# Optimization experiments

Measured on AMD Instinct MI355X. Metric: run time of the kernel, lower is better.

Reference implementation:

```python
import jax, jax.numpy as jnp
import numpy as np

N_NODES = 50000
N_EDGES = 800000
NUM_GRAPHS = 256
F_IN = 64        # num_features (per-head out dim == in dim in this module)
HEADS = 4        # n_heads1
OUT_DIM = 128    # output_dim
HC = HEADS * F_IN
NEG_SLOPE = 0.2  # GATConv leaky_relu slope
EPS = 1e-5       # GraphNorm eps


def setup_inputs() -> dict:
    key = jax.random.key(0)
    ks = jax.random.split(key, 12)
    s = lambda k, shape, fan: (jax.random.normal(k, shape, jnp.float32) / np.sqrt(fan).astype(np.float32))
    return {
        "x": jax.random.normal(ks[0], (N_NODES, F_IN), jnp.float32),
        "edge_index": jax.random.randint(ks[1], (2, N_EDGES), 0, N_NODES),
        "batch": jnp.sort(jax.random.randint(ks[2], (N_NODES,), 0, NUM_GRAPHS)),
        # GATConv params
        "lin_w": s(ks[3], (HC, F_IN), F_IN),
        "att_src": s(ks[4], (HEADS, F_IN), F_IN),
        "att_dst": s(ks[5], (HEADS, F_IN), F_IN),
        "gat_bias": jnp.zeros((HC,), jnp.float32),
        # GraphNorm params
        "gn_weight": jnp.ones((HC,), jnp.float32),
        "gn_bias": jnp.zeros((HC,), jnp.float32),
        "gn_mean_scale": jnp.ones((HC,), jnp.float32),
        # fc_g1 / out heads
        "fc1_w": s(ks[6], (OUT_DIM, HC), HC), "fc1_b": jnp.zeros((OUT_DIM,), jnp.float32),
        "out_w": s(ks[7], (1, OUT_DIM), OUT_DIM), "out_b": jnp.zeros((1,), jnp.float32),
        # GlobalAttention gate_nn: Linear(HC,16) -> ReLU -> Linear(16,1) -> Sigmoid
        "att1_w": s(ks[8], (16, HC), HC), "att1_b": jnp.zeros((16,), jnp.float32),
        "att2_w": s(ks[9], (1, 16), 16), "att2_b": jnp.zeros((1,), jnp.float32),
    }


def _gat_conv(x, edge_index, lin_w, att_src, att_dst, gat_bias):
    """PyG GATConv with add_self_loops=True, concat heads. Returns (out [N,HC], alpha [E+N,H])."""
    N = x.shape[0]
    xh = (x @ lin_w.T).reshape(N, HEADS, F_IN)                 # [N,H,C]
    a_src = (xh * att_src[None]).sum(-1)                        # [N,H]
    a_dst = (xh * att_dst[None]).sum(-1)                        # [N,H]
    loops = jnp.arange(N)
    src = jnp.concatenate([edge_index[0], loops])               # [E+N]
    dst = jnp.concatenate([edge_index[1], loops])
    alpha = jax.nn.leaky_relu(a_src[src] + a_dst[dst], NEG_SLOPE)  # [E+N,H]
    # segment softmax over incoming edges of each dst node (self-loops guarantee non-empty)
    amax = jax.ops.segment_max(alpha, dst, num_segments=N)
    alpha = jnp.exp(alpha - amax[dst])
    denom = jax.ops.segment_sum(alpha, dst, num_segments=N)
    alpha = alpha / (denom[dst] + 1e-16)
    msg = xh[src] * alpha[:, :, None]                           # [E+N,H,C]
    out = jax.ops.segment_sum(msg, dst, num_segments=N).reshape(N, HC) + gat_bias
    return out, alpha


def _graph_norm(x, batch, weight, bias, mean_scale):
    ones = jnp.ones((x.shape[0],), x.dtype)
    cnt = jnp.maximum(jax.ops.segment_sum(ones, batch, num_segments=NUM_GRAPHS), 1.0)[:, None]
    mean = jax.ops.segment_sum(x, batch, num_segments=NUM_GRAPHS) / cnt
    sub = x - mean[batch] * mean_scale
    var = jax.ops.segment_sum(sub * sub, batch, num_segments=NUM_GRAPHS) / cnt
    return weight * sub / jnp.sqrt(var + EPS)[batch] + bias


def _global_attention(x, batch, att1_w, att1_b, att2_w, att2_b):
    gate = jax.nn.sigmoid(jax.nn.relu(x @ att1_w.T + att1_b) @ att2_w.T + att2_b)  # [N,1]
    gmax = jax.ops.segment_max(gate, batch, num_segments=NUM_GRAPHS)
    gate = jnp.exp(gate - gmax[batch])
    gden = jax.ops.segment_sum(gate, batch, num_segments=NUM_GRAPHS)
    gate = gate / (gden[batch] + 1e-16)
    return jax.ops.segment_sum(gate * x, batch, num_segments=NUM_GRAPHS)  # [G,HC]


def reference(x, edge_index, batch, lin_w, att_src, att_dst, gat_bias,
              gn_weight, gn_bias, gn_mean_scale, fc1_w, fc1_b, out_w, out_b,
              att1_w, att1_b, att2_w, att2_b):
    x2, alpha = _gat_conv(x, edge_index, lin_w, att_src, att_dst, gat_bias)
    h = _graph_norm(x2, batch, gn_weight, gn_bias, gn_mean_scale)
    h = jax.nn.relu(h)                                # node_dropout = identity (eval)
    pooled = _global_attention(h, batch, att1_w, att1_b, att2_w, att2_b)
    h = jax.nn.relu(pooled @ fc1_w.T + fc1_b)          # dropout = identity (eval)
    out = jax.nn.sigmoid(h @ out_w.T + out_b)          # [G,1]
    return out, alpha
```

## Files before the change

### kernel.cpp

```cpp
#include <hip/hip_runtime.h>
#include <hip/hip_fp16.h>
#include <math.h>

#define NN 50000
#define NE 800000
#define NG 256
#define NEG_SLOPE 0.2f
#define GEPS 1e-5f
#define CHUNK 64
#define NB 196
#define CAP 6144
#define NAB 261
#define EPB 3072
#define NLINB 782
#define ABLK 3321
#define GMAX 512

typedef _Float16 f16x8 __attribute__((ext_vector_type(8)));
typedef _Float16 f16x4 __attribute__((ext_vector_type(4)));
typedef float f32x4 __attribute__((ext_vector_type(4)));
typedef float f32x2 __attribute__((ext_vector_type(2)));

__device__ __forceinline__ float lrelu(float v){ return v > 0.f ? v : NEG_SLOPE * v; }

__global__ __launch_bounds__(256) void k_misc(const float* __restrict__ lin_w,
                                              _Float16* __restrict__ wh,
                                              const float* __restrict__ att1_w,
                                              _Float16* __restrict__ a1w,
                                              const int* __restrict__ batch,
                                              int* __restrict__ goff,
                                              int* __restrict__ gcnt,
                                              int* __restrict__ bucket_cnt) {
  int b = blockIdx.x, tid = threadIdx.x;
  if (b == 0) {
    if (tid < NB) bucket_cnt[tid] = 0;
    int g = tid;
    int lo = 0, hi = NN;
    while (lo < hi) { int mid = (lo + hi) >> 1; if (batch[mid] < g) lo = mid + 1; else hi = mid; }
    int start = lo;
    lo = 0; hi = NN;
    while (lo < hi) { int mid = (lo + hi) >> 1; if (batch[mid] < g + 1) lo = mid + 1; else hi = mid; }
    goff[g] = start;
    gcnt[g] = lo - start;
  } else if (b <= 16) {
    int i0 = (b - 1) * 1024 + tid * 4;
    float4 f = *(const float4*)&lin_w[i0];
    f16x4 h4;
    h4[0] = (_Float16)f.x; h4[1] = (_Float16)f.y; h4[2] = (_Float16)f.z; h4[3] = (_Float16)f.w;
    *(f16x4*)&wh[i0] = h4;
  } else {
    int i0 = (b - 17) * 1024 + tid * 4;
    float4 f = *(const float4*)&att1_w[i0];
    f16x4 h4;
    h4[0] = (_Float16)f.x; h4[1] = (_Float16)f.y; h4[2] = (_Float16)f.z; h4[3] = (_Float16)f.w;
    *(f16x4*)&a1w[i0] = h4;
  }
}

__device__ __forceinline__ void lin_body(char* smem,
                                         const float* __restrict__ x,
                                         const _Float16* __restrict__ wh,
                                         const float* __restrict__ att_src,
                                         const float* __restrict__ att_dst,
                                         unsigned char* __restrict__ xh8,
                                         float* __restrict__ a_src_n,
                                         float* __restrict__ a_dst_n) {
  unsigned char* s_f8 = (unsigned char*)smem;
  int w = threadIdx.x >> 6, lane = threadIdx.x & 63;
  int nb = blockIdx.x * 64 + w * 16;
  if (nb >= NN) return;
  int am = lane & 15, quad = lane >> 4;
  int wb = w * 4096;

  const float* xr = x + (size_t)(nb + am) * 64 + quad * 8;
  float4 f0 = *(const float4*)(xr);
  float4 f1 = *(const float4*)(xr + 4);
  float4 f2 = *(const float4*)(xr + 32);
  float4 f3 = *(const float4*)(xr + 36);
  f16x8 a0, a1;
  a0[0] = (_Float16)f0.x; a0[1] = (_Float16)f0.y; a0[2] = (_Float16)f0.z; a0[3] = (_Float16)f0.w;
  a0[4] = (_Float16)f1.x; a0[5] = (_Float16)f1.y; a0[6] = (_Float16)f1.z; a0[7] = (_Float16)f1.w;
  a1[0] = (_Float16)f2.x; a1[1] = (_Float16)f2.y; a1[2] = (_Float16)f2.z; a1[3] = (_Float16)f2.w;
  a1[4] = (_Float16)f3.x; a1[5] = (_Float16)f3.y; a1[6] = (_Float16)f3.z; a1[7] = (_Float16)f3.w;

  f32x4 acc[16];
#pragma unroll
  for (int ct = 0; ct < 16; ct++) acc[ct] = (f32x4){0.f, 0.f, 0.f, 0.f};

#pragma unroll
  for (int ct = 0; ct < 16; ct++) {
    const _Float16* wbp = wh + (size_t)(ct * 16 + am) * 64 + quad * 8;
    f16x8 b0 = *(const f16x8*)(wbp);
    f16x8 b1 = *(const f16x8*)(wbp + 32);
    acc[ct] = __builtin_amdgcn_mfma_f32_16x16x32_f16(a0, b0, acc[ct], 0, 0, 0);
    acc[ct] = __builtin_amdgcn_mfma_f32_16x16x32_f16(a1, b1, acc[ct], 0, 0, 0);
  }

  float ps[4][4], pd[4][4];
#pragma unroll
  for (int r = 0; r < 4; r++)
#pragma unroll
    for (int h = 0; h < 4; h++) { ps[r][h] = 0.f; pd[r][h] = 0.f; }
#pragma unroll
  for (int ct = 0; ct < 16; ct++) {
    int c = ct * 16 + am;
    float av = att_src[c];
    float dv = att_dst[c];
    int h = ct >> 2;
#pragma unroll
    for (int r = 0; r < 4; r++) {
      float v = acc[ct][r];
      ps[r][h] += v * av;
      pd[r][h] += v * dv;
    }
  }
#pragma unroll
  for (int r = 0; r < 4; r++)
#pragma unroll
    for (int h = 0; h < 4; h++) {
      float s = ps[r][h], d = pd[r][h];
#pragma unroll
      for (int o = 1; o < 16; o <<= 1) {
        s += __shfl_xor(s, o, 64);
        d += __shfl_xor(d, o, 64);
      }
      if (am == 0) {
        int node = nb + quad * 4 + r;
        a_src_n[node * 4 + h] = s;
        a_dst_n[node * 4 + h] = d;
      }
    }

#pragma unroll
  for (int r = 0; r < 4; r++) {
    uint4 u;
    int t;
    t = __builtin_amdgcn_cvt_pk_fp8_f32(acc[0][r],  acc[1][r],  0, 0);
    t = __builtin_amdgcn_cvt_pk_fp8_f32(acc[2][r],  acc[3][r],  t, 1);
    u.x = (unsigned)t;
    t = __builtin_amdgcn_cvt_pk_fp8_f32(acc[4][r],  acc[5][r],  0, 0);
    t = __builtin_amdgcn_cvt_pk_fp8_f32(acc[6][r],  acc[7][r],  t, 1);
    u.y = (unsigned)t;
    t = __builtin_amdgcn_cvt_pk_fp8_f32(acc[8][r],  acc[9][r],  0, 0);
    t = __builtin_amdgcn_cvt_pk_fp8_f32(acc[10][r], acc[11][r], t, 1);
    u.z = (unsigned)t;
    t = __builtin_amdgcn_cvt_pk_fp8_f32(acc[12][r], acc[13][r], 0, 0);
    t = __builtin_amdgcn_cvt_pk_fp8_f32(acc[14][r], acc[15][r], t, 1);
    u.w = (unsigned)t;
    *(uint4*)&s_f8[wb + (quad * 4 + r) * 256 + am * 16] = u;
  }
#pragma unroll
  for (int p = 0; p < 4; p++) {
    uint4 u = *(const uint4*)&s_f8[wb + p * 1024 + lane * 16];
    *(uint4*)&xh8[(size_t)nb * 256 + p * 1024 + lane * 16] = u;
  }
}

__device__ __forceinline__ void binA_body(char* smem, int b,
                                          const int* __restrict__ ei,
                                          int* __restrict__ bucket_cnt,
                                          int2* __restrict__ ebuf) {
  int2* sorted = (int2*)smem;
  int*  hist   = (int*)(smem + 24576);
  int*  lbase  = (int*)(smem + 25360);
  int*  cur    = (int*)(smem + 26144);
  int*  runb   = (int*)(smem + 26928);
  int*  wsum   = (int*)(smem + 27712);
  int tid = threadIdx.x, lane = tid & 63, wid = tid >> 6;
  int e0 = b * EPB, e1 = min(e0 + EPB, NE);
  int n = e1 - e0;
  bool full = (e0 + EPB <= NE);

  int dd[12];
  if (full) {
#pragma unroll
    for (int r = 0; r < 3; r++) {
      int e = e0 + r * 1024 + tid * 4;
      int4 v = *(const int4*)&ei[NE + e];
      dd[r * 4 + 0] = v.x; dd[r * 4 + 1] = v.y;
      dd[r * 4 + 2] = v.z; dd[r * 4 + 3] = v.w;
    }
  } else {
#pragma unroll
    for (int r = 0; r < 3; r++)
#pragma unroll
      for (int k = 0; k < 4; k++) {
        int e = e0 + r * 1024 + tid * 4 + k;
        dd[r * 4 + k] = (e < e1) ? ei[NE + e] : -1;
      }
  }
  if (tid < NB) hist[tid] = 0;
  __syncthreads();
#pragma unroll
  for (int q = 0; q < 12; q++)
    if (dd[q] >= 0) atomicAdd(&hist[dd[q] >> 8], 1);
  __syncthreads();
  {
    int v = (tid < NB) ? hist[tid] : 0;
    int s = v;
#pragma unroll
    for (int o = 1; o < 64; o <<= 1) { int t = __shfl_up(s, o, 64); if (lane >= o) s += t; }
    if (lane == 63) wsum[wid] = s;
    __syncthreads();
    int wbase = 0;
    for (int k = 0; k < wid; k++) wbase += wsum[k];
    if (tid < NB) {
      int ex = wbase + s - v;
      lbase[tid] = ex;
      cur[tid] = ex;
      runb[tid] = atomicAdd(&bucket_cnt[tid], v);
    }
  }
  __syncthreads();
  int ss[12];
  if (full) {
#pragma unroll
    for (int r = 0; r < 3; r++) {
      int e = e0 + r * 1024 + tid * 4;
      int4 v = *(const int4*)&ei[e];
      ss[r * 4 + 0] = v.x; ss[r * 4 + 1] = v.y;
      ss[r * 4 + 2] = v.z; ss[r * 4 + 3] = v.w;
    }
  } else {
#pragma unroll
    for (int r = 0; r < 3; r++)
#pragma unroll
      for (int k = 0; k < 4; k++) {
        int e = e0 + r * 1024 + tid * 4 + k;
        ss[r * 4 + k] = (e < e1) ? ei[e] : 0;
      }
  }
#pragma unroll
  for (int q = 0; q < 12; q++) {
    int d = dd[q];
    if (d >= 0) {
      int lp = atomicAdd(&cur[d >> 8], 1);
      sorted[lp] = make_int2(d, ss[q]);
    }
  }
  __syncthreads();
  for (int i = tid; i < n; i += 256) {
    int2 e = sorted[i];
    int bk = e.x >> 8;
    int slot = runb[bk] + (i - lbase[bk]);
    if (slot < CAP) ebuf[(size_t)bk * CAP + slot] = e;
  }
}

__global__ __launch_bounds__(256) void k_linbin(const float* __restrict__ x,
                                                const _Float16* __restrict__ wh,
                                                const float* __restrict__ att_src,
                                                const float* __restrict__ att_dst,
                                                unsigned char* __restrict__ xh8,
                                                float* __restrict__ a_src_n,
                                                float* __restrict__ a_dst_n,
                                                const int* __restrict__ ei,
                                                int* __restrict__ bucket_cnt,
                                                int2* __restrict__ ebuf) {
  __shared__ __align__(16) char smem[27744];
  if (blockIdx.x < NLINB)
    lin_body(smem, x, wh, att_src, att_dst, xh8, a_src_n, a_dst_n);
  else
    binA_body(smem, blockIdx.x - NLINB, ei, bucket_cnt, ebuf);
}

__global__ __launch_bounds__(256) void k_binB(const int2* __restrict__ ebuf,
                                              const int* __restrict__ bucket_cnt,
                                              int* __restrict__ deg,
                                              int* __restrict__ offs,
                                              int* __restrict__ src_list) {
  __shared__ int hist[256];
  __shared__ int cur[256];
  __shared__ int wsum[4];
  __shared__ int bbase[NB];
  int b = blockIdx.x, tid = threadIdx.x, lane = tid & 63, wid = tid >> 6;
  {
    int v = (tid < NB) ? min(bucket_cnt[tid], CAP) : 0;
    int s = v;
#pragma unroll
    for (int o = 1; o < 64; o <<= 1) { int t = __shfl_up(s, o, 64); if (lane >= o) s += t; }
    if (lane == 63) wsum[wid] = s;
    __syncthreads();
    int wbase = 0;
    for (int k = 0; k < wid; k++) wbase += wsum[k];
    if (tid < NB) bbase[tid] = wbase + s - v;
  }
  __syncthreads();
  int cnt = min(bucket_cnt[b], CAP);
  int base = bbase[b];
  const int2* seg = ebuf + (size_t)b * CAP;
  hist[tid] = 0;
  __syncthreads();
  for (int i = tid; i < cnt; i += 256) atomicAdd(&hist[seg[i].x & 255], 1);
  __syncthreads();
  int v = hist[tid];
  int s = v;
#pragma unroll
  for (int o = 1; o < 64; o <<= 1) { int t = __shfl_up(s, o, 64); if (lane >= o) s += t; }
  if (lane == 63) wsum[wid] = s;
  __syncthreads();
  int wbase = 0;
  for (int k = 0; k < wid; k++) wbase += wsum[k];
  int excl = wbase + s - v;
  int node = b * 256 + tid;
  if (node < NN) {
    deg[node] = v;
    offs[node] = base + excl;
  }
  cur[tid] = excl;
  __syncthreads();
  for (int i = tid; i < cnt; i += 256) {
    int2 e = seg[i];
    int pos = base + atomicAdd(&cur[e.x & 255], 1);
    src_list[pos] = e.y;
  }
}

__global__ __launch_bounds__(64) void k_gat(const unsigned char* __restrict__ xh8,
                                            const float* __restrict__ a_src_n,
                                            const float* __restrict__ a_dst_n,
                                            const int* __restrict__ offs,
                                            const int* __restrict__ deg_arr,
                                            const int* __restrict__ src_list,
                                            const float* __restrict__ gat_bias,
                                            __half* __restrict__ x2h,
                                            float* __restrict__ den_inv) {
  __shared__ __align__(16) float s_al[CHUNK * 4];
  __shared__ int s_src[CHUNK];
  __shared__ __half s_tr[256];
  int n = blockIdx.x, lane = threadIdx.x;
  int off = offs[n], dg = deg_arr[n], cnt = dg + 1;
  float4 ad = *(const float4*)&a_dst_n[n * 4];
  int h = lane & 3;
  unsigned loff = 4u * (unsigned)lane;
  float acc0 = 0.f, acc1 = 0.f, acc2 = 0.f, acc3 = 0.f;

  if (cnt <= 64) {
    float e0 = 0.f, e1 = 0.f, e2 = 0.f, e3 = 0.f;
    if (lane < cnt) {
      int src = (lane < dg) ? src_list[off + lane] : n;
      float4 as = *(const float4*)&a_src_n[src * 4];
      e0 = __expf(lrelu(as.x + ad.x));
      e1 = __expf(lrelu(as.y + ad.y));
      e2 = __expf(lrelu(as.z + ad.z));
      e3 = __expf(lrelu(as.w + ad.w));
      s_src[lane] = src;
    }
    float s0 = e0, s1 = e1, s2 = e2, s3 = e3;
#pragma unroll
    for (int o = 32; o >= 1; o >>= 1) {
      s0 += __shfl_xor(s0, o, 64);
      s1 += __shfl_xor(s1, o, 64);
      s2 += __shfl_xor(s2, o, 64);
      s3 += __shfl_xor(s3, o, 64);
    }
    float i0 = 1.f / (s0 + 1e-16f), i1 = 1.f / (s1 + 1e-16f);
    float i2 = 1.f / (s2 + 1e-16f), i3 = 1.f / (s3 + 1e-16f);
    if (lane == 0) *(float4*)&den_inv[n * 4] = make_float4(i0, i1, i2, i3);
    if (lane < cnt) {
      s_al[lane * 4 + 0] = e0 * i0;
      s_al[lane * 4 + 1] = e1 * i1;
      s_al[lane * 4 + 2] = e2 * i2;
      s_al[lane * 4 + 3] = e3 * i3;
    }
    __syncthreads();
    int j = 0;
    for (; j + 4 <= cnt; j += 4) {
      unsigned oA = ((unsigned)s_src[j] << 8) + loff;
      unsigned oB = ((unsigned)s_src[j + 1] << 8) + loff;
      unsigned oC = ((unsigned)s_src[j + 2] << 8) + loff;
      unsigned oD = ((unsigned)s_src[j + 3] << 8) + loff;
      unsigned rA = *(const unsigned*)&xh8[oA];
      unsigned rB = *(const unsigned*)&xh8[oB];
      unsigned rC = *(const unsigned*)&xh8[oC];
      unsigned rD = *(const unsigned*)&xh8[oD];
      float aA = s_al[j * 4 + h], aB = s_al[(j + 1) * 4 + h];
      float aC = s_al[(j + 2) * 4 + h], aD = s_al[(j + 3) * 4 + h];
      f32x2 lA = __builtin_amdgcn_cvt_pk_f32_fp8((int)rA, 0);
      f32x2 hA = __builtin_amdgcn_cvt_pk_f32_fp8((int)rA, 1);
      f32x2 lB = __builtin_amdgcn_cvt_pk_f32_fp8((int)rB, 0);
      f32x2 hB = __builtin_amdgcn_cvt_pk_f32_fp8((int)rB, 1);
      f32x2 lC = __builtin_amdgcn_cvt_pk_f32_fp8((int)rC, 0);
      f32x2 hC = __builtin_amdgcn_cvt_pk_f32_fp8((int)rC, 1);
      f32x2 lD = __builtin_amdgcn_cvt_pk_f32_fp8((int)rD, 0);
      f32x2 hD = __builtin_amdgcn_cvt_pk_f32_fp8((int)rD, 1);
      acc0 += aA * lA[0] + aB * lB[0] + aC * lC[0] + aD * lD[0];
      acc1 += aA * lA[1] + aB * lB[1] + aC * lC[1] + aD * lD[1];
      acc2 += aA * hA[0] + aB * hB[0] + aC * hC[0] + aD * hD[0];
      acc3 += aA * hA[1] + aB * hB[1] + aC * hC[1] + aD * hD[1];
    }
    for (; j < cnt; j++) {
      unsigned oA = ((unsigned)s_src[j] << 8) + loff;
      unsigned rA = *(const unsigned*)&xh8[oA];
      float aA = s_al[j * 4 + h];
      f32x2 lA = __builtin_amdgcn_cvt_pk_f32_fp8((int)rA, 0);
      f32x2 hA = __builtin_amdgcn_cvt_pk_f32_fp8((int)rA, 1);
      acc0 += aA * lA[0];
      acc1 += aA * lA[1];
      acc2 += aA * hA[0];
      acc3 += aA * hA[1];
    }
  } else {
    float s0 = 0.f, s1 = 0.f, s2 = 0.f, s3 = 0.f;
    for (int j = lane; j < cnt; j += 64) {
      int src = (j < dg) ? src_list[off + j] : n;
      float4 as = *(const float4*)&a_src_n[src * 4];
      s0 += __expf(lrelu(as.x + ad.x));
      s1 += __expf(lrelu(as.y + ad.y));
      s2 += __expf(lrelu(as.z + ad.z));
      s3 += __expf(lrelu(as.w + ad.w));
    }
#pragma unroll
    for (int o = 32; o >= 1; o >>= 1) {
      s0 += __shfl_xor(s0, o, 64);
      s1 += __shfl_xor(s1, o, 64);
      s2 += __shfl_xor(s2, o, 64);
      s3 += __shfl_xor(s3, o, 64);
    }
    float i0 = 1.f / (s0 + 1e-16f), i1 = 1.f / (s1 + 1e-16f);
    float i2 = 1.f / (s2 + 1e-16f), i3 = 1.f / (s3 + 1e-16f);
    if (lane == 0) *(float4*)&den_inv[n * 4] = make_float4(i0, i1, i2, i3);
    for (int cb = 0; cb < cnt; cb += CHUNK) {
      int clen = min(CHUNK, cnt - cb);
      for (int j = lane; j < clen; j += 64) {
        int jj = cb + j;
        int src = (jj < dg) ? src_list[off + jj] : n;
        float4 as = *(const float4*)&a_src_n[src * 4];
        s_src[j] = src;
        s_al[j * 4 + 0] = __expf(lrelu(as.x + ad.x)) * i0;
        s_al[j * 4 + 1] = __expf(lrelu(as.y + ad.y)) * i1;
        s_al[j * 4 + 2] = __expf(lrelu(as.z + ad.z)) * i2;
        s_al[j * 4 + 3] = __expf(lrelu(as.w + ad.w)) * i3;
      }
      __syncthreads();
      for (int j = 0; j < clen; j++) {
        unsigned oA = ((unsigned)s_src[j] << 8) + loff;
        unsigned rA = *(const unsigned*)&xh8[oA];
        float aA = s_al[j * 4 + h];
        f32x2 lA = __builtin_amdgcn_cvt_pk_f32_fp8((int)rA, 0);
        f32x2 hA = __builtin_amdgcn_cvt_pk_f32_fp8((int)rA, 1);
        acc0 += aA * lA[0];
        acc1 += aA * lA[1];
        acc2 += aA * hA[0];
        acc3 += aA * hA[1];
      }
      __syncthreads();
    }
  }

  int cb0 = (lane & 3) * 64 + (lane >> 2);
  s_tr[cb0 +  0] = __float2half(acc0 + gat_bias[cb0 +  0]);
  s_tr[cb0 + 16] = __float2half(acc1 + gat_bias[cb0 + 16]);
  s_tr[cb0 + 32] = __float2half(acc2 + gat_bias[cb0 + 32]);
  s_tr[cb0 + 48] = __float2half(acc3 + gat_bias[cb0 + 48]);
  __syncthreads();
  uint2 u = *(const uint2*)&s_tr[4 * lane];
  *(uint2*)&x2h[(size_t)n * 256 + 4 * lane] = u;
}

__global__ __launch_bounds__(256) void k_tail(const int* __restrict__ ei,
                                              const float* __restrict__ a_src_n,
                                              const float* __restrict__ a_dst_n,
                                              const float* __restrict__ den_inv,
                                              float* __restrict__ alpha_out,
                                              const int* __restrict__ gcnt,
                                              const int* __restrict__ goff,
                                              const float* __restrict__ gn_w,
                                              const float* __restrict__ gn_b,
                                              const float* __restrict__ gn_ms,
                                              const __half* __restrict__ x2h,
                                              const _Float16* __restrict__ a1w,
                                              const float* __restrict__ att1_b,
                                              const float* __restrict__ att2_w,
                                              const float* __restrict__ att2_b,
                                              const float* __restrict__ fc1_w,
                                              const float* __restrict__ fc1_b,
                                              const float* __restrict__ out_w,
                                              const float* __restrict__ out_b,
                                              float* __restrict__ outp) {
  if (blockIdx.x >= NG) {
    int idx = (blockIdx.x - NG) * 256 + threadIdx.x;
    if (idx >= NE + NN) return;
    int s, d;
    if (idx < NE) { s = ei[idx]; d = ei[NE + idx]; }
    else          { s = idx - NE; d = s; }
    float4 as = *(const float4*)&a_src_n[s * 4];
    float4 ad = *(const float4*)&a_dst_n[d * 4];
    float4 iv = *(const float4*)&den_inv[d * 4];
    float4 a;
    a.x = __expf(lrelu(as.x + ad.x)) * iv.x;
    a.y = __expf(lrelu(as.y + ad.y)) * iv.y;
    a.z = __expf(lrelu(as.z + ad.z)) * iv.z;
    a.w = __expf(lrelu(as.w + ad.w)) * iv.w;
    *(float4*)&alpha_out[(size_t)idx * 4] = a;
    return;
  }

  __shared__ __align__(16) float s_sc[256];
  __shared__ __align__(16) float s_sh[256];
  __shared__ float s_gate[GMAX];
  __shared__ __align__(16) float pool_s[256];
  __shared__ float hred[128];
  __shared__ float red[4];
  int g = blockIdx.x, tid = threadIdx.x, lane = tid & 63, wid = tid >> 6;
  int cnt = gcnt[g], start = goff[g];

  {
    int c = tid;
    const __half* p = x2h + (size_t)start * 256 + c;
    float S = 0.f, S2 = 0.f;
    int i = 0;
    for (; i + 7 < cnt; i += 8) {
      float v0 = __half2float(p[(size_t)(i + 0) * 256]);
      float v1 = __half2float(p[(size_t)(i + 1) * 256]);
      float v2 = __half2float(p[(size_t)(i + 2) * 256]);
      float v3 = __half2float(p[(size_t)(i + 3) * 256]);
      float v4 = __half2float(p[(size_t)(i + 4) * 256]);
      float v5 = __half2float(p[(size_t)(i + 5) * 256]);
      float v6 = __half2float(p[(size_t)(i + 6) * 256]);
      float v7 = __half2float(p[(size_t)(i + 7) * 256]);
      S  += ((v0 + v1) + (v2 + v3)) + ((v4 + v5) + (v6 + v7));
      S2 += ((v0 * v0 + v1 * v1) + (v2 * v2 + v3 * v3)) +
            ((v4 * v4 + v5 * v5) + (v6 * v6 + v7 * v7));
    }
    for (; i < cnt; i++) { float v = __half2float(p[(size_t)i * 256]); S += v; S2 += v * v; }
    float fc = fmaxf((float)cnt, 1.f);
    float mean = S / fc;
    float mm = mean * gn_ms[c];
    float var = fmaxf(S2 / fc - 2.f * mm * mean + mm * mm, 0.f);
    float sc = gn_w[c] / sqrtf(var + GEPS);
    s_sc[c] = sc;
    s_sh[c] = gn_b[c] - sc * mm;
  }
  __syncthreads();

  int am = lane & 15, quad = lane >> 4;
  float b1 = att1_b[am], w2 = att2_w[am], b2 = att2_b[0];
  const _Float16* bp = a1w + am * 256 + quad * 8;
  for (int i0 = wid * 16; i0 < cnt; i0 += 64) {
    int node = start + i0 + am;
    if (node > NN - 1) node = NN - 1;
    const __half* xp = x2h + (size_t)node * 256 + quad * 8;
    f32x4 ga = (f32x4){0.f, 0.f, 0.f, 0.f};
#pragma unroll
    for (int kb = 0; kb < 8; kb++) {
      f16x8 xv = *(const f16x8*)(xp + kb * 32);
      int cb = quad * 8 + kb * 32;
      float4 sc0 = *(const float4*)&s_sc[cb];
      float4 sc1 = *(const float4*)&s_sc[cb + 4];
      float4 sh0 = *(const float4*)&s_sh[cb];
      float4 sh1 = *(const float4*)&s_sh[cb + 4];
      f16x8 a;
      a[0] = (_Float16)fmaxf(sc0.x * (float)xv[0] + sh0.x, 0.f);
      a[1] = (_Float16)fmaxf(sc0.y * (float)xv[1] + sh0.y, 0.f);
      a[2] = (_Float16)fmaxf(sc0.z * (float)xv[2] + sh0.z, 0.f);
      a[3] = (_Float16)fmaxf(sc0.w * (float)xv[3] + sh0.w, 0.f);
      a[4] = (_Float16)fmaxf(sc1.x * (float)xv[4] + sh1.x, 0.f);
      a[5] = (_Float16)fmaxf(sc1.y * (float)xv[5] + sh1.y, 0.f);
      a[6] = (_Float16)fmaxf(sc1.z * (float)xv[6] + sh1.z, 0.f);
      a[7] = (_Float16)fmaxf(sc1.w * (float)xv[7] + sh1.w, 0.f);
      f16x8 b = *(const f16x8*)(bp + kb * 32);
      ga = __builtin_amdgcn_mfma_f32_16x16x32_f16(a, b, ga, 0, 0, 0);
    }
#pragma unroll
    for (int r = 0; r < 4; r++) {
      float t = w2 * fmaxf(ga[r] + b1, 0.f);
#pragma unroll
      for (int o = 1; o < 16; o <<= 1) t += __shfl_xor(t, o, 64);
      if (am == 0) {
        int li = i0 + quad * 4 + r;
        if (li < cnt && li < GMAX)
          s_gate[li] = __expf(1.f / (1.f + __expf(-(t + b2))));
      }
    }
  }
  __syncthreads();

  float ls = 0.f;
  for (int i = tid; i < cnt; i += 256) ls += s_gate[i];
#pragma unroll
  for (int o = 32; o >= 1; o >>= 1) ls += __shfl_xor(ls, o, 64);
  if (lane == 0) red[wid] = ls;
  __syncthreads();
  float rden = 1.f / (red[0] + red[1] + red[2] + red[3] + 1e-16f);

  {
    int c = tid;
    float sc = s_sc[c], sh = s_sh[c];
    const __half* p = x2h + (size_t)start * 256 + c;
    float a0 = 0.f, a1_ = 0.f, a2 = 0.f, a3 = 0.f;
    float a4 = 0.f, a5 = 0.f, a6 = 0.f, a7 = 0.f;
    int i = 0;
    for (; i + 7 < cnt; i += 8) {
      float v0 = __half2float(p[(size_t)(i + 0) * 256]);
      float v1 = __half2float(p[(size_t)(i + 1) * 256]);
      float v2 = __half2float(p[(size_t)(i + 2) * 256]);
      float v3 = __half2float(p[(size_t)(i + 3) * 256]);
      float v4 = __half2float(p[(size_t)(i + 4) * 256]);
      float v5 = __half2float(p[(size_t)(i + 5) * 256]);
      float v6 = __half2float(p[(size_t)(i + 6) * 256]);
      float v7 = __half2float(p[(size_t)(i + 7) * 256]);
      a0 += s_gate[i + 0] * fmaxf(sc * v0 + sh, 0.f);
      a1_ += s_gate[i + 1] * fmaxf(sc * v1 + sh, 0.f);
      a2 += s_gate[i + 2] * fmaxf(sc * v2 + sh, 0.f);
      a3 += s_gate[i + 3] * fmaxf(sc * v3 + sh, 0.f);
      a4 += s_gate[i + 4] * fmaxf(sc * v4 + sh, 0.f);
      a5 += s_gate[i + 5] * fmaxf(sc * v5 + sh, 0.f);
      a6 += s_gate[i + 6] * fmaxf(sc * v6 + sh, 0.f);
      a7 += s_gate[i + 7] * fmaxf(sc * v7 + sh, 0.f);
    }
    for (; i < cnt; i++)
      a0 += s_gate[i] * fmaxf(sc * __half2float(p[(size_t)i * 256]) + sh, 0.f);
    pool_s[c] = ((((a0 + a1_) + (a2 + a3)) + ((a4 + a5) + (a6 + a7)))) * rden;
  }
  __syncthreads();

  float4 psv = *(const float4*)&pool_s[4 * lane];
  for (int j0 = 0; j0 < 32; j0++) {
    int j = wid * 32 + j0;
    float4 w = *(const float4*)&fc1_w[j * 256 + 4 * lane];
    float d = w.x * psv.x + w.y * psv.y + w.z * psv.z + w.w * psv.w;
#pragma unroll
    for (int o = 32; o >= 1; o >>= 1) d += __shfl_xor(d, o, 64);
    if (lane == 0) hred[j] = fmaxf(d + fc1_b[j], 0.f) * out_w[j];
  }
  __syncthreads();
  if (tid < 128) {
    float v = hred[tid];
#pragma unroll
    for (int o = 32; o >= 1; o >>= 1) v += __shfl_xor(v, o, 64);
    if (lane == 0) red[wid] = v;
  }
  __syncthreads();
  if (tid == 0) outp[g] = 1.f / (1.f + __expf(-(red[0] + red[1] + out_b[0])));
}

extern "C" void kernel_launch(void* const* d_in, const int* in_sizes, int n_in,
                              void* d_out, int out_size, void* d_ws, size_t ws_size,
                              hipStream_t stream) {
  const float* x        = (const float*)d_in[0];
  const int*   ei       = (const int*)d_in[1];
  const int*   batch    = (const int*)d_in[2];
  const float* lin_w    = (const float*)d_in[3];
  const float* att_src  = (const float*)d_in[4];
  const float* att_dst  = (const float*)d_in[5];
  const float* gat_bias = (const float*)d_in[6];
  const float* gn_w     = (const float*)d_in[7];
  const float* gn_b     = (const float*)d_in[8];
  const float* gn_ms    = (const float*)d_in[9];
  const float* fc1_w    = (const float*)d_in[10];
  const float* fc1_b    = (const float*)d_in[11];
  const float* out_w    = (const float*)d_in[12];
  const float* out_b    = (const float*)d_in[13];
  const float* att1_w   = (const float*)d_in[14];
  const float* att1_b   = (const float*)d_in[15];
  const float* att2_w   = (const float*)d_in[16];
  const float* att2_b   = (const float*)d_in[17];

  float* outp  = (float*)d_out;
  float* alpha = outp + NG;

  char* wsb = (char*)d_ws;
  size_t o = 0;
  auto A = [&](size_t bytes) -> char* {
    char* p = wsb + o;
    o += (bytes + 255) & ~(size_t)255;
    return p;
  };
  unsigned char* xh8 = (unsigned char*)A((size_t)NN * 256);
  __half*   x2h      = (__half*)A((size_t)NN * 256 * 2);
  _Float16* wh       = (_Float16*)A((size_t)256 * 64 * 2);
  _Float16* a1w      = (_Float16*)A((size_t)16 * 256 * 2);
  float* a_src_n  = (float*)A((size_t)NN * 4 * 4);
  float* a_dst_n  = (float*)A((size_t)NN * 4 * 4);
  float* den_inv  = (float*)A((size_t)NN * 4 * 4);
  int*   deg      = (int*)A((size_t)NN * 4);
  int*   gcnt     = (int*)A((size_t)NG * 4);
  int*   offs     = (int*)A((size_t)NN * 4);
  int*   goff     = (int*)A((size_t)NG * 4);
  int*   src_list = (int*)A((size_t)NE * 4);
  int2*  ebuf     = (int2*)A((size_t)NB * CAP * 8);
  int*   bucket_cnt  = (int*)A((size_t)NB * 4);

  k_misc<<<21, 256, 0, stream>>>(lin_w, wh, att1_w, a1w, batch, goff, gcnt, bucket_cnt);
  k_linbin<<<NLINB + NAB, 256, 0, stream>>>(x, wh, att_src, att_dst, xh8, a_src_n, a_dst_n,
                                            ei, bucket_cnt, ebuf);
  k_binB<<<NB, 256, 0, stream>>>(ebuf, bucket_cnt, deg, offs, src_list);
  k_gat<<<NN, 64, 0, stream>>>(xh8, a_src_n, a_dst_n, offs, deg, src_list,
                               gat_bias, x2h, den_inv);
  k_tail<<<NG + ABLK, 256, 0, stream>>>(ei, a_src_n, a_dst_n, den_inv, alpha,
                                        gcnt, goff, gn_w, gn_b, gn_ms, x2h,
                                        a1w, att1_b, att2_w, att2_b, fc1_w, fc1_b,
                                        out_w, out_b, outp);
}
```

Measured before the change: 234.7 us.

## Write attention coefficients directly from GAT kernel via stored edge indices

The binning pass now stores the original edge index instead of the source node, and the GAT aggregation kernel looks up the source through the edge array and writes the normalized alpha straight to its output slot. This removes the separate alpha-recompute blocks in the tail kernel and the den_inv buffer, avoiding a second pass over all edges with gathers of a_src, a_dst and den_inv. The cost is an extra dependent gather (ei[eidx]) per edge in the GAT kernel and scattered float4 writes of alpha in edge order.

```diff
diff --git a/kernel.cpp b/kernel.cpp
--- a/kernel.cpp
+++ b/kernel.cpp
@@ -13,7 +13,6 @@
 #define NAB 261
 #define EPB 3072
 #define NLINB 782
-#define ABLK 3321
 #define GMAX 512
 
 typedef _Float16 f16x8 __attribute__((ext_vector_type(8)));
@@ -212,30 +211,14 @@
     }
   }
   __syncthreads();
-  int ss[12];
-  if (full) {
-#pragma unroll
-    for (int r = 0; r < 3; r++) {
-      int e = e0 + r * 1024 + tid * 4;
-      int4 v = *(const int4*)&ei[e];
-      ss[r * 4 + 0] = v.x; ss[r * 4 + 1] = v.y;
-      ss[r * 4 + 2] = v.z; ss[r * 4 + 3] = v.w;
-    }
-  } else {
-#pragma unroll
-    for (int r = 0; r < 3; r++)
-#pragma unroll
-      for (int k = 0; k < 4; k++) {
-        int e = e0 + r * 1024 + tid * 4 + k;
-        ss[r * 4 + k] = (e < e1) ? ei[e] : 0;
-      }
-  }
 #pragma unroll
   for (int q = 0; q < 12; q++) {
     int d = dd[q];
     if (d >= 0) {
+      int r = q >> 2, k = q & 3;
+      int eidx = e0 + r * 1024 + tid * 4 + k;
       int lp = atomicAdd(&cur[d >> 8], 1);
-      sorted[lp] = make_int2(d, ss[q]);
+      sorted[lp] = make_int2(d, eidx);
     }
   }
   __syncthreads();
@@ -322,9 +305,10 @@
                                             const int* __restrict__ offs,
                                             const int* __restrict__ deg_arr,
                                             const int* __restrict__ src_list,
+                                            const int* __restrict__ ei,
                                             const float* __restrict__ gat_bias,
                                             __half* __restrict__ x2h,
-                                            float* __restrict__ den_inv) {
+                                            float* __restrict__ alpha_out) {
   __shared__ __align__(16) float s_al[CHUNK * 4];
   __shared__ int s_src[CHUNK];
   __shared__ __half s_tr[256];
@@ -337,8 +321,11 @@
 
   if (cnt <= 64) {
     float e0 = 0.f, e1 = 0.f, e2 = 0.f, e3 = 0.f;
+    int eidx = 0;
     if (lane < cnt) {
-      int src = (lane < dg) ? src_list[off + lane] : n;
+      int src;
+      if (lane < dg) { eidx = src_list[off + lane]; src = ei[eidx]; }
+      else           { eidx = NE + n;               src = n; }
       float4 as = *(const float4*)&a_src_n[src * 4];
       e0 = __expf(lrelu(as.x + ad.x));
       e1 = __expf(lrelu(as.y + ad.y));
@@ -356,12 +343,13 @@
     }
     float i0 = 1.f / (s0 + 1e-16f), i1 = 1.f / (s1 + 1e-16f);
     float i2 = 1.f / (s2 + 1e-16f), i3 = 1.f / (s3 + 1e-16f);
-    if (lane == 0) *(float4*)&den_inv[n * 4] = make_float4(i0, i1, i2, i3);
     if (lane < cnt) {
-      s_al[lane * 4 + 0] = e0 * i0;
-      s_al[lane * 4 + 1] = e1 * i1;
-      s_al[lane * 4 + 2] = e2 * i2;
-      s_al[lane * 4 + 3] = e3 * i3;
+      float a0v = e0 * i0, a1v = e1 * i1, a2v = e2 * i2, a3v = e3 * i3;
+      *(float4*)&alpha_out[(size_t)eidx * 4] = make_float4(a0v, a1v, a2v, a3v);
+      s_al[lane * 4 + 0] = a0v;
+      s_al[lane * 4 + 1] = a1v;
+      s_al[lane * 4 + 2] = a2v;
+      s_al[lane * 4 + 3] = a3v;
     }
     __syncthreads();
     int j = 0;
@@ -403,7 +391,7 @@
   } else {
     float s0 = 0.f, s1 = 0.f, s2 = 0.f, s3 = 0.f;
     for (int j = lane; j < cnt; j += 64) {
-      int src = (j < dg) ? src_list[off + j] : n;
+      int src = (j < dg) ? ei[src_list[off + j]] : n;
       float4 as = *(const float4*)&a_src_n[src * 4];
       s0 += __expf(lrelu(as.x + ad.x));
       s1 += __expf(lrelu(as.y + ad.y));
@@ -419,18 +407,24 @@
     }
     float i0 = 1.f / (s0 + 1e-16f), i1 = 1.f / (s1 + 1e-16f);
     float i2 = 1.f / (s2 + 1e-16f), i3 = 1.f / (s3 + 1e-16f);
-    if (lane == 0) *(float4*)&den_inv[n * 4] = make_float4(i0, i1, i2, i3);
     for (int cb = 0; cb < cnt; cb += CHUNK) {
       int clen = min(CHUNK, cnt - cb);
       for (int j = lane; j < clen; j += 64) {
         int jj = cb + j;
-        int src = (jj < dg) ? src_list[off + jj] : n;
+        int eidx, src;
+        if (jj < dg) { eidx = src_list[off + jj]; src = ei[eidx]; }
+        else         { eidx = NE + n;             src = n; }
         float4 as = *(const float4*)&a_src_n[src * 4];
+        float a0v = __expf(lrelu(as.x + ad.x)) * i0;
+        float a1v = __expf(lrelu(as.y + ad.y)) * i1;
+        float a2v = __expf(lrelu(as.z + ad.z)) * i2;
+        float a3v = __expf(lrelu(as.w + ad.w)) * i3;
+        *(float4*)&alpha_out[(size_t)eidx * 4] = make_float4(a0v, a1v, a2v, a3v);
         s_src[j] = src;
-        s_al[j * 4 + 0] = __expf(lrelu(as.x + ad.x)) * i0;
-        s_al[j * 4 + 1] = __expf(lrelu(as.y + ad.y)) * i1;
-        s_al[j * 4 + 2] = __expf(lrelu(as.z + ad.z)) * i2;
-        s_al[j * 4 + 3] = __expf(lrelu(as.w + ad.w)) * i3;
+        s_al[j * 4 + 0] = a0v;
+        s_al[j * 4 + 1] = a1v;
+        s_al[j * 4 + 2] = a2v;
+        s_al[j * 4 + 3] = a3v;
       }
       __syncthreads();
       for (int j = 0; j < clen; j++) {
@@ -458,12 +452,7 @@
   *(uint2*)&x2h[(size_t)n * 256 + 4 * lane] = u;
 }
 
-__global__ __launch_bounds__(256) void k_tail(const int* __restrict__ ei,
-                                              const float* __restrict__ a_src_n,
-                                              const float* __restrict__ a_dst_n,
-                                              const float* __restrict__ den_inv,
-                                              float* __restrict__ alpha_out,
-                                              const int* __restrict__ gcnt,
+__global__ __launch_bounds__(256) void k_tail(const int* __restrict__ gcnt,
                                               const int* __restrict__ goff,
                                               const float* __restrict__ gn_w,
                                               const float* __restrict__ gn_b,
@@ -478,24 +467,6 @@
                                               const float* __restrict__ out_w,
                                               const float* __restrict__ out_b,
                                               float* __restrict__ outp) {
-  if (blockIdx.x >= NG) {
-    int idx = (blockIdx.x - NG) * 256 + threadIdx.x;
-    if (idx >= NE + NN) return;
-    int s, d;
-    if (idx < NE) { s = ei[idx]; d = ei[NE + idx]; }
-    else          { s = idx - NE; d = s; }
-    float4 as = *(const float4*)&a_src_n[s * 4];
-    float4 ad = *(const float4*)&a_dst_n[d * 4];
-    float4 iv = *(const float4*)&den_inv[d * 4];
-    float4 a;
-    a.x = __expf(lrelu(as.x + ad.x)) * iv.x;
-    a.y = __expf(lrelu(as.y + ad.y)) * iv.y;
-    a.z = __expf(lrelu(as.z + ad.z)) * iv.z;
-    a.w = __expf(lrelu(as.w + ad.w)) * iv.w;
-    *(float4*)&alpha_out[(size_t)idx * 4] = a;
-    return;
-  }
-
   __shared__ __align__(16) float s_sc[256];
   __shared__ __align__(16) float s_sh[256];
   __shared__ float s_gate[GMAX];
@@ -673,7 +644,6 @@
   _Float16* a1w      = (_Float16*)A((size_t)16 * 256 * 2);
   float* a_src_n  = (float*)A((size_t)NN * 4 * 4);
   float* a_dst_n  = (float*)A((size_t)NN * 4 * 4);
-  float* den_inv  = (float*)A((size_t)NN * 4 * 4);
   int*   deg      = (int*)A((size_t)NN * 4);
   int*   gcnt     = (int*)A((size_t)NG * 4);
   int*   offs     = (int*)A((size_t)NN * 4);
@@ -686,10 +656,9 @@
   k_linbin<<<NLINB + NAB, 256, 0, stream>>>(x, wh, att_src, att_dst, xh8, a_src_n, a_dst_n,
                                             ei, bucket_cnt, ebuf);
   k_binB<<<NB, 256, 0, stream>>>(ebuf, bucket_cnt, deg, offs, src_list);
-  k_gat<<<NN, 64, 0, stream>>>(xh8, a_src_n, a_dst_n, offs, deg, src_list,
-                               gat_bias, x2h, den_inv);
-  k_tail<<<NG + ABLK, 256, 0, stream>>>(ei, a_src_n, a_dst_n, den_inv, alpha,
-                                        gcnt, goff, gn_w, gn_b, gn_ms, x2h,
-                                        a1w, att1_b, att2_w, att2_b, fc1_w, fc1_b,
-                                        out_w, out_b, outp);
-}
+  k_gat<<<NN, 64, 0, stream>>>(xh8, a_src_n, a_dst_n, offs, deg, src_list, ei,
+                               gat_bias, x2h, alpha);
+  k_tail<<<NG, 256, 0, stream>>>(gcnt, goff, gn_w, gn_b, gn_ms, x2h,
+                                 a1w, att1_b, att2_w, att2_b, fc1_w, fc1_b,
+                                 out_w, out_b, outp);
+}
```

Result: slower. 241.4 us (+2.9%).

## Gather 16-byte fp8 rows per lane in GAT aggregation and split alpha kernel

Applied to the files above, without the earlier changes.

The GAT aggregation now assigns each 16-lane group to a different edge. Each lane loads 16 contiguous fp8 bytes (one uint4) of the source row and keeps 16 accumulators, where before every lane did a 4-byte load per edge. Partial sums are reduced across the four edge groups with xor shuffles, and edge counts are padded to multiples of four using zero-weight dummy entries. The intent is wider, fewer memory transactions per gathered row, at the cost of more registers and a cross-lane reduction. The alpha-output work is also moved out of k_tail into its own kernel launch, adding one launch.

```diff
diff --git a/kernel.cpp b/kernel.cpp
--- a/kernel.cpp
+++ b/kernel.cpp
@@ -331,11 +331,14 @@
   int n = blockIdx.x, lane = threadIdx.x;
   int off = offs[n], dg = deg_arr[n], cnt = dg + 1;
   float4 ad = *(const float4*)&a_dst_n[n * 4];
-  int h = lane & 3;
-  unsigned loff = 4u * (unsigned)lane;
-  float acc0 = 0.f, acc1 = 0.f, acc2 = 0.f, acc3 = 0.f;
+  int m = lane & 15, eg = lane >> 4;
+  unsigned coff = (unsigned)m * 16u;
+  float acc[16];
+#pragma unroll
+  for (int t = 0; t < 16; t++) acc[t] = 0.f;
 
   if (cnt <= 64) {
+    int cnt4 = (cnt + 3) & ~3;
     float e0 = 0.f, e1 = 0.f, e2 = 0.f, e3 = 0.f;
     if (lane < cnt) {
       int src = (lane < dg) ? src_list[off + lane] : n;
@@ -345,6 +348,9 @@
       e2 = __expf(lrelu(as.z + ad.z));
       e3 = __expf(lrelu(as.w + ad.w));
       s_src[lane] = src;
+    } else if (lane < cnt4) {
+      s_src[lane] = n;
+      *(float4*)&s_al[lane * 4] = make_float4(0.f, 0.f, 0.f, 0.f);
     }
     float s0 = e0, s1 = e1, s2 = e2, s3 = e3;
 #pragma unroll
@@ -364,41 +370,20 @@
       s_al[lane * 4 + 3] = e3 * i3;
     }
     __syncthreads();
-    int j = 0;
-    for (; j + 4 <= cnt; j += 4) {
-      unsigned oA = ((unsigned)s_src[j] << 8) + loff;
-      unsigned oB = ((unsigned)s_src[j + 1] << 8) + loff;
-      unsigned oC = ((unsigned)s_src[j + 2] << 8) + loff;
-      unsigned oD = ((unsigned)s_src[j + 3] << 8) + loff;
-      unsigned rA = *(const unsigned*)&xh8[oA];
-      unsigned rB = *(const unsigned*)&xh8[oB];
-      unsigned rC = *(const unsigned*)&xh8[oC];
-      unsigned rD = *(const unsigned*)&xh8[oD];
-      float aA = s_al[j * 4 + h], aB = s_al[(j + 1) * 4 + h];
-      float aC = s_al[(j + 2) * 4 + h], aD = s_al[(j + 3) * 4 + h];
-      f32x2 lA = __builtin_amdgcn_cvt_pk_f32_fp8((int)rA, 0);
-      f32x2 hA = __builtin_amdgcn_cvt_pk_f32_fp8((int)rA, 1);
-      f32x2 lB = __builtin_amdgcn_cvt_pk_f32_fp8((int)rB, 0);
-      f32x2 hB = __builtin_amdgcn_cvt_pk_f32_fp8((int)rB, 1);
-      f32x2 lC = __builtin_amdgcn_cvt_pk_f32_fp8((int)rC, 0);
-      f32x2 hC = __builtin_amdgcn_cvt_pk_f32_fp8((int)rC, 1);
-      f32x2 lD = __builtin_amdgcn_cvt_pk_f32_fp8((int)rD, 0);
-      f32x2 hD = __builtin_amdgcn_cvt_pk_f32_fp8((int)rD, 1);
-      acc0 += aA * lA[0] + aB * lB[0] + aC * lC[0] + aD * lD[0];
-      acc1 += aA * lA[1] + aB * lB[1] + aC * lC[1] + aD * lD[1];
-      acc2 += aA * hA[0] + aB * hB[0] + aC * hC[0] + aD * hD[0];
-      acc3 += aA * hA[1] + aB * hB[1] + aC * hC[1] + aD * hD[1];
-    }
-    for (; j < cnt; j++) {
-      unsigned oA = ((unsigned)s_src[j] << 8) + loff;
-      unsigned rA = *(const unsigned*)&xh8[oA];
-      float aA = s_al[j * 4 + h];
-      f32x2 lA = __builtin_amdgcn_cvt_pk_f32_fp8((int)rA, 0);
-      f32x2 hA = __builtin_amdgcn_cvt_pk_f32_fp8((int)rA, 1);
-      acc0 += aA * lA[0];
-      acc1 += aA * lA[1];
-      acc2 += aA * hA[0];
-      acc3 += aA * hA[1];
+    for (int j = 0; j < cnt4; j += 4) {
+      int jj = j + eg;
+      unsigned o8 = ((unsigned)s_src[jj] << 8) + coff;
+      uint4 rv = *(const uint4*)&xh8[o8];
+      float4 al = *(const float4*)&s_al[jj * 4];
+      f32x2 p;
+      p = __builtin_amdgcn_cvt_pk_f32_fp8((int)rv.x, 0); acc[0]  += al.x * p[0]; acc[1]  += al.x * p[1];
+      p = __builtin_amdgcn_cvt_pk_f32_fp8((int)rv.x, 1); acc[2]  += al.x * p[0]; acc[3]  += al.x * p[1];
+      p = __builtin_amdgcn_cvt_pk_f32_fp8((int)rv.y, 0); acc[4]  += al.y * p[0]; acc[5]  += al.y * p[1];
+      p = __builtin_amdgcn_cvt_pk_f32_fp8((int)rv.y, 1); acc[6]  += al.y * p[0]; acc[7]  += al.y * p[1];
+      p = __builtin_amdgcn_cvt_pk_f32_fp8((int)rv.z, 0); acc[8]  += al.z * p[0]; acc[9]  += al.z * p[1];
+      p = __builtin_amdgcn_cvt_pk_f32_fp8((int)rv.z, 1); acc[10] += al.z * p[0]; acc[11] += al.z * p[1];
+      p = __builtin_amdgcn_cvt_pk_f32_fp8((int)rv.w, 0); acc[12] += al.w * p[0]; acc[13] += al.w * p[1];
+      p = __builtin_amdgcn_cvt_pk_f32_fp8((int)rv.w, 1); acc[14] += al.w * p[0]; acc[15] += al.w * p[1];
     }
   } else {
     float s0 = 0.f, s1 = 0.f, s2 = 0.f, s3 = 0.f;
@@ -422,48 +407,81 @@
     if (lane == 0) *(float4*)&den_inv[n * 4] = make_float4(i0, i1, i2, i3);
     for (int cb = 0; cb < cnt; cb += CHUNK) {
       int clen = min(CHUNK, cnt - cb);
-      for (int j = lane; j < clen; j += 64) {
+      int clen4 = (clen + 3) & ~3;
+      for (int j = lane; j < clen4; j += 64) {
         int jj = cb + j;
-        int src = (jj < dg) ? src_list[off + jj] : n;
-        float4 as = *(const float4*)&a_src_n[src * 4];
-        s_src[j] = src;
-        s_al[j * 4 + 0] = __expf(lrelu(as.x + ad.x)) * i0;
-        s_al[j * 4 + 1] = __expf(lrelu(as.y + ad.y)) * i1;
-        s_al[j * 4 + 2] = __expf(lrelu(as.z + ad.z)) * i2;
-        s_al[j * 4 + 3] = __expf(lrelu(as.w + ad.w)) * i3;
+        if (j < clen) {
+          int src = (jj < dg) ? src_list[off + jj] : n;
+          float4 as = *(const float4*)&a_src_n[src * 4];
+          s_src[j] = src;
+          s_al[j * 4 + 0] = __expf(lrelu(as.x + ad.x)) * i0;
+          s_al[j * 4 + 1] = __expf(lrelu(as.y + ad.y)) * i1;
+          s_al[j * 4 + 2] = __expf(lrelu(as.z + ad.z)) * i2;
+          s_al[j * 4 + 3] = __expf(lrelu(as.w + ad.w)) * i3;
+        } else {
+          s_src[j] = n;
+          *(float4*)&s_al[j * 4] = make_float4(0.f, 0.f, 0.f, 0.f);
+        }
       }
       __syncthreads();
-      for (int j = 0; j < clen; j++) {
-        unsigned oA = ((unsigned)s_src[j] << 8) + loff;
-        unsigned rA = *(const unsigned*)&xh8[oA];
-        float aA = s_al[j * 4 + h];
-        f32x2 lA = __builtin_amdgcn_cvt_pk_f32_fp8((int)rA, 0);
-        f32x2 hA = __builtin_amdgcn_cvt_pk_f32_fp8((int)rA, 1);
-        acc0 += aA * lA[0];
-        acc1 += aA * lA[1];
-        acc2 += aA * hA[0];
-        acc3 += aA * hA[1];
+      for (int j = 0; j < clen4; j += 4) {
+        int jj = j + eg;
+        unsigned o8 = ((unsigned)s_src[jj] << 8) + coff;
+        uint4 rv = *(const uint4*)&xh8[o8];
+        float4 al = *(const float4*)&s_al[jj * 4];
+        f32x2 p;
+        p = __builtin_amdgcn_cvt_pk_f32_fp8((int)rv.x, 0); acc[0]  += al.x * p[0]; acc[1]  += al.x * p[1];
+        p = __builtin_amdgcn_cvt_pk_f32_fp8((int)rv.x, 1); acc[2]  += al.x * p[0]; acc[3]  += al.x * p[1];
+        p = __builtin_amdgcn_cvt_pk_f32_fp8((int)rv.y, 0); acc[4]  += al.y * p[0]; acc[5]  += al.y * p[1];
+        p = __builtin_amdgcn_cvt_pk_f32_fp8((int)rv.y, 1); acc[6]  += al.y * p[0]; acc[7]  += al.y * p[1];
+        p = __builtin_amdgcn_cvt_pk_f32_fp8((int)rv.z, 0); acc[8]  += al.z * p[0]; acc[9]  += al.z * p[1];
+        p = __builtin_amdgcn_cvt_pk_f32_fp8((int)rv.z, 1); acc[10] += al.z * p[0]; acc[11] += al.z * p[1];
+        p = __builtin_amdgcn_cvt_pk_f32_fp8((int)rv.w, 0); acc[12] += al.w * p[0]; acc[13] += al.w * p[1];
+        p = __builtin_amdgcn_cvt_pk_f32_fp8((int)rv.w, 1); acc[14] += al.w * p[0]; acc[15] += al.w * p[1];
       }
       __syncthreads();
     }
   }
 
-  int cb0 = (lane & 3) * 64 + (lane >> 2);
-  s_tr[cb0 +  0] = __float2half(acc0 + gat_bias[cb0 +  0]);
-  s_tr[cb0 + 16] = __float2half(acc1 + gat_bias[cb0 + 16]);
-  s_tr[cb0 + 32] = __float2half(acc2 + gat_bias[cb0 + 32]);
-  s_tr[cb0 + 48] = __float2half(acc3 + gat_bias[cb0 + 48]);
+#pragma unroll
+  for (int t = 0; t < 16; t++) {
+    acc[t] += __shfl_xor(acc[t], 16, 64);
+    acc[t] += __shfl_xor(acc[t], 32, 64);
+  }
+  if (lane < 16) {
+#pragma unroll
+    for (int t = 0; t < 16; t++) {
+      int c = t * 16 + lane;
+      s_tr[c] = __float2half(acc[t] + gat_bias[c]);
+    }
+  }
   __syncthreads();
   uint2 u = *(const uint2*)&s_tr[4 * lane];
   *(uint2*)&x2h[(size_t)n * 256 + 4 * lane] = u;
 }
 
-__global__ __launch_bounds__(256) void k_tail(const int* __restrict__ ei,
-                                              const float* __restrict__ a_src_n,
-                                              const float* __restrict__ a_dst_n,
-                                              const float* __restrict__ den_inv,
-                                              float* __restrict__ alpha_out,
-                                              const int* __restrict__ gcnt,
+__global__ __launch_bounds__(256) void k_alpha(const int* __restrict__ ei,
+                                               const float* __restrict__ a_src_n,
+                                               const float* __restrict__ a_dst_n,
+                                               const float* __restrict__ den_inv,
+                                               float* __restrict__ alpha_out) {
+  int idx = blockIdx.x * 256 + threadIdx.x;
+  if (idx >= NE + NN) return;
+  int s, d;
+  if (idx < NE) { s = ei[idx]; d = ei[NE + idx]; }
+  else          { s = idx - NE; d = s; }
+  float4 as = *(const float4*)&a_src_n[s * 4];
+  float4 ad = *(const float4*)&a_dst_n[d * 4];
+  float4 iv = *(const float4*)&den_inv[d * 4];
+  float4 a;
+  a.x = __expf(lrelu(as.x + ad.x)) * iv.x;
+  a.y = __expf(lrelu(as.y + ad.y)) * iv.y;
+  a.z = __expf(lrelu(as.z + ad.z)) * iv.z;
+  a.w = __expf(lrelu(as.w + ad.w)) * iv.w;
+  *(float4*)&alpha_out[(size_t)idx * 4] = a;
+}
+
+__global__ __launch_bounds__(256) void k_tail(const int* __restrict__ gcnt,
                                               const int* __restrict__ goff,
                                               const float* __restrict__ gn_w,
                                               const float* __restrict__ gn_b,
@@ -478,24 +496,6 @@
                                               const float* __restrict__ out_w,
                                               const float* __restrict__ out_b,
                                               float* __restrict__ outp) {
-  if (blockIdx.x >= NG) {
-    int idx = (blockIdx.x - NG) * 256 + threadIdx.x;
-    if (idx >= NE + NN) return;
-    int s, d;
-    if (idx < NE) { s = ei[idx]; d = ei[NE + idx]; }
-    else          { s = idx - NE; d = s; }
-    float4 as = *(const float4*)&a_src_n[s * 4];
-    float4 ad = *(const float4*)&a_dst_n[d * 4];
-    float4 iv = *(const float4*)&den_inv[d * 4];
-    float4 a;
-    a.x = __expf(lrelu(as.x + ad.x)) * iv.x;
-    a.y = __expf(lrelu(as.y + ad.y)) * iv.y;
-    a.z = __expf(lrelu(as.z + ad.z)) * iv.z;
-    a.w = __expf(lrelu(as.w + ad.w)) * iv.w;
-    *(float4*)&alpha_out[(size_t)idx * 4] = a;
-    return;
-  }
-
   __shared__ __align__(16) float s_sc[256];
   __shared__ __align__(16) float s_sh[256];
   __shared__ float s_gate[GMAX];
@@ -688,8 +688,8 @@
   k_binB<<<NB, 256, 0, stream>>>(ebuf, bucket_cnt, deg, offs, src_list);
   k_gat<<<NN, 64, 0, stream>>>(xh8, a_src_n, a_dst_n, offs, deg, src_list,
                                gat_bias, x2h, den_inv);
-  k_tail<<<NG + ABLK, 256, 0, stream>>>(ei, a_src_n, a_dst_n, den_inv, alpha,
-                                        gcnt, goff, gn_w, gn_b, gn_ms, x2h,
-                                        a1w, att1_b, att2_w, att2_b, fc1_w, fc1_b,
-                                        out_w, out_b, outp);
-}
+  k_alpha<<<ABLK, 256, 0, stream>>>(ei, a_src_n, a_dst_n, den_inv, alpha);
+  k_tail<<<NG, 256, 0, stream>>>(gcnt, goff, gn_w, gn_b, gn_ms, x2h,
+                                 a1w, att1_b, att2_w, att2_b, fc1_w, fc1_b,
+                                 out_w, out_b, outp);
+}
```

Result: slower. 251.4 us (+7.1%).
